# Optimization experiments

Hardware: AMD Instinct MI355X
Metric: run time of the kernel (lower is better)

The kernel has to match this reference:

```python
import jax, jax.numpy as jnp
import numpy as np

D = 512       # d_model
H = 8         # n_heads
HD = D // H   # head_dim
LYR = 4       # number_of_layers
PMT = 20      # pmt_len
L = 2048      # decode / target length (src_len - pmt_len)
BS = 1
DOUT = 3      # d_output (3 coding classes)
DFF = 4 * D
EPS = 1e-5


def layer_norm(x, g, b):
    m = jnp.mean(x, axis=-1, keepdims=True)
    v = jnp.mean((x - m) ** 2, axis=-1, keepdims=True)
    return (x - m) * jax.lax.rsqrt(v + EPS) * g + b


def rope(x):
    # x: (b, h, s, hd); half-split rotary with base 10000, positions = arange(s)
    half = x.shape[-1] // 2
    pos = jnp.arange(x.shape[2], dtype=jnp.float32)
    inv_freq = 1.0 / (10000.0 ** (jnp.arange(half, dtype=jnp.float32) / half))
    ang = pos[:, None] * inv_freq[None, :]          # (s, half)
    cos = jnp.cos(ang)[None, None]                  # (1,1,s,half)
    sin = jnp.sin(ang)[None, None]
    x1, x2 = x[..., :half], x[..., half:]
    return jnp.concatenate([x1 * cos - x2 * sin, x1 * sin + x2 * cos], axis=-1)


def mha(xq, xkv, wqkv, bqkv, wo, bo, key_mask, causal):
    # xq: (b, sq, D), xkv: (b, sk, D); key_mask: (b, sk) with 1=valid
    b, sq, _ = xq.shape
    sk = xkv.shape[1]
    q = xq @ wqkv[:, :D] + bqkv[:D]
    kv = xkv @ wqkv[:, D:] + bqkv[D:]
    k, v = kv[..., :D], kv[..., D:]
    q = q.reshape(b, sq, H, HD).transpose(0, 2, 1, 3)   # (b,h,sq,hd)
    k = k.reshape(b, sk, H, HD).transpose(0, 2, 1, 3)
    v = v.reshape(b, sk, H, HD).transpose(0, 2, 1, 3)
    q = rope(q)
    k = rope(k)
    scores = jnp.einsum('bhqd,bhkd->bhqk', q, k) / jnp.sqrt(jnp.float32(HD))
    scores = scores + jnp.where(key_mask[:, None, None, :] > 0, 0.0, -1e9)
    if causal:
        cm = jnp.tril(jnp.ones((sq, sk), dtype=bool))
        scores = jnp.where(cm[None, None], scores, -1e9)
    attn = jax.nn.softmax(scores, axis=-1)
    out = jnp.einsum('bhqk,bhkd->bhqd', attn, v)
    out = out.transpose(0, 2, 1, 3).reshape(b, sq, D)
    return out @ wo + bo


def setup_inputs() -> dict:
    key = jax.random.key(0)
    ks = jax.random.split(key, 16)
    s = 0.02
    p = lambda i, shape: jax.random.normal(ks[i], shape, jnp.float32) * s
    return {
        'trg_inputs': jax.random.normal(ks[0], (BS, L, DOUT), jnp.float32),
        'src_rep': jax.random.normal(ks[1], (BS, PMT + L, D), jnp.float32),
        'src_mask': jnp.ones((BS, L), jnp.float32),
        'emb_w': p(2, (DOUT, D)), 'emb_b': jnp.zeros((D,), jnp.float32),
        'sa_wqkv': p(3, (LYR, D, 3 * D)), 'sa_bqkv': jnp.zeros((LYR, 3 * D), jnp.float32),
        'sa_wo': p(4, (LYR, D, D)), 'sa_bo': jnp.zeros((LYR, D), jnp.float32),
        'ca_wqkv': p(5, (LYR, D, 3 * D)), 'ca_bqkv': jnp.zeros((LYR, 3 * D), jnp.float32),
        'ca_wo': p(6, (LYR, D, D)), 'ca_bo': jnp.zeros((LYR, D), jnp.float32),
        'ffn_w1': p(7, (LYR, D, DFF)), 'ffn_b1': jnp.zeros((LYR, DFF), jnp.float32),
        'ffn_w2': p(8, (LYR, DFF, D)), 'ffn_b2': jnp.zeros((LYR, D), jnp.float32),
        'ln_g': jnp.ones((LYR, 3, D), jnp.float32), 'ln_b': jnp.zeros((LYR, 3, D), jnp.float32),
        'lnf_g': jnp.ones((D,), jnp.float32), 'lnf_b': jnp.zeros((D,), jnp.float32),
        'gen_w': p(9, (D, DOUT)), 'gen_b': jnp.zeros((DOUT,), jnp.float32),
    }


def reference(trg_inputs, src_rep, src_mask, emb_w, emb_b, sa_wqkv, sa_bqkv, sa_wo, sa_bo,
              ca_wqkv, ca_bqkv, ca_wo, ca_bo, ffn_w1, ffn_b1, ffn_w2, ffn_b2,
              ln_g, ln_b, lnf_g, lnf_b, gen_w, gen_b):
    srb = src_rep[:, PMT:, :]                       # (bs, L, D)
    x = trg_inputs @ emb_w + emb_b                  # (bs, L, D)
    trg_mask = src_mask                             # parallel mode: trg_mask = src_mask
    for li in range(LYR):
        h = layer_norm(x, ln_g[li, 0], ln_b[li, 0])
        x = x + mha(h, h, sa_wqkv[li], sa_bqkv[li], sa_wo[li], sa_bo[li], trg_mask, causal=True)
        h = layer_norm(x, ln_g[li, 1], ln_b[li, 1])
        x = x + mha(h, srb, ca_wqkv[li], ca_bqkv[li], ca_wo[li], ca_bo[li], src_mask, causal=False)
        h = layer_norm(x, ln_g[li, 2], ln_b[li, 2])
        x = x + (jax.nn.relu(h @ ffn_w1[li] + ffn_b1[li]) @ ffn_w2[li] + ffn_b2[li])
    x = layer_norm(x, lnf_g, lnf_b)
    return x @ gen_w + gen_b                        # logits (bs, L, 3)
```

## Files before the change

### kernel.cpp

```cpp
#include <hip/hip_runtime.h>
#include <hip/hip_bf16.h>

#define SEQ 2048
#define DM 512
#define NHEAD 8
#define HDIM 64
#define DFFN 2048
#define PMTN 20

typedef __bf16 bf16x8 __attribute__((ext_vector_type(8)));
typedef float f32x4 __attribute__((ext_vector_type(4)));
typedef unsigned short u16x8 __attribute__((ext_vector_type(8)));

__device__ __forceinline__ float wave_sum(float v) {
#pragma unroll
  for (int off = 32; off; off >>= 1) v += __shfl_xor(v, off);
  return v;
}

__device__ __forceinline__ unsigned short f2b(float x) {
  __hip_bfloat16 h = __float2bfloat16(x);
  return *(unsigned short*)&h;
}

__device__ __forceinline__ void gll16(const __hip_bfloat16* g, __hip_bfloat16* l) {
  __builtin_amdgcn_global_load_lds(
      (const __attribute__((address_space(1))) unsigned int*)(g),
      (__attribute__((address_space(3))) unsigned int*)(l), 16, 0, 0);
}

__global__ __launch_bounds__(256) void embed_kernel(
    const float* __restrict__ trg, const float* __restrict__ w,
    const float* __restrict__ b, float* __restrict__ X) {
  int idx = blockIdx.x * 256 + threadIdx.x;
  int r = idx >> 9, c = idx & 511;
  float t0 = trg[r * 3 + 0], t1 = trg[r * 3 + 1], t2 = trg[r * 3 + 2];
  X[idx] = t0 * w[c] + t1 * w[512 + c] + t2 * w[1024 + c] + b[c];
}

__global__ __launch_bounds__(256) void cast_bf16_kernel(
    const float* __restrict__ in, __hip_bfloat16* __restrict__ out) {
  int i = blockIdx.x * 256 + threadIdx.x;
  out[i] = __float2bfloat16(in[i]);
}

__global__ __launch_bounds__(256) void rope_table_kernel(float2* __restrict__ rt) {
  int idx = blockIdx.x * 256 + threadIdx.x;
  int row = idx >> 5, i = idx & 31;
  float inv = __expf(-(float)i * (9.210340371976184f / 32.f));
  float sn, cs;
  sincosf((float)row * inv, &sn, &cs);
  rt[idx] = make_float2(cs, sn);
}

__global__ __launch_bounds__(256) void mbias_kernel(
    const float* __restrict__ mask, float* __restrict__ mb,
    int* __restrict__ mtflag) {
  int i = blockIdx.x * 256 + threadIdx.x;
  bool masked = !(mask[i] > 0.f);
  mb[i] = masked ? -8.0e9f : 0.f;
  unsigned long long any = __ballot(masked);
  if ((threadIdx.x & 63) == 0) mtflag[i >> 6] = (any != 0ull) ? 1 : 0;
}

__global__ __launch_bounds__(256) void ln_bf16_kernel(
    const float* __restrict__ x, const float* __restrict__ g,
    const float* __restrict__ b, __hip_bfloat16* __restrict__ o) {
  int row = blockIdx.x * 4 + (threadIdx.x >> 6);
  int lane = threadIdx.x & 63;
  const float* xr = x + (long)row * DM;
  float v[8];
  float s = 0.f;
#pragma unroll
  for (int j = 0; j < 8; j++) { v[j] = xr[lane + 64 * j]; s += v[j]; }
  s = wave_sum(s);
  float mean = s * (1.f / DM);
  float q = 0.f;
#pragma unroll
  for (int j = 0; j < 8; j++) { float d = v[j] - mean; q += d * d; }
  q = wave_sum(q);
  float r = rsqrtf(q * (1.f / DM) + 1e-5f);
  __hip_bfloat16* orow = o + (long)row * DM;
#pragma unroll
  for (int j = 0; j < 8; j++) {
    int c = lane + 64 * j;
    orow[c] = __float2bfloat16((v[j] - mean) * r * g[c] + b[c]);
  }
}

__global__ __launch_bounds__(256) void ln_f32_kernel(
    const float* __restrict__ x, const float* __restrict__ g,
    const float* __restrict__ b, float* __restrict__ o) {
  int row = blockIdx.x * 4 + (threadIdx.x >> 6);
  int lane = threadIdx.x & 63;
  const float* xr = x + (long)row * DM;
  float v[8];
  float s = 0.f;
#pragma unroll
  for (int j = 0; j < 8; j++) { v[j] = xr[lane + 64 * j]; s += v[j]; }
  s = wave_sum(s);
  float mean = s * (1.f / DM);
  float q = 0.f;
#pragma unroll
  for (int j = 0; j < 8; j++) { float d = v[j] - mean; q += d * d; }
  q = wave_sum(q);
  float r = rsqrtf(q * (1.f / DM) + 1e-5f);
  float* orow = o + (long)row * DM;
#pragma unroll
  for (int j = 0; j < 8; j++) {
    int c = lane + 64 * j;
    orow[c] = (v[j] - mean) * r * g[c] + b[c];
  }
}

__global__ __launch_bounds__(256) void transpose_layer_kernel(
    const float* __restrict__ wqkv, const float* __restrict__ wo,
    const float* __restrict__ cwqkv, const float* __restrict__ cwo,
    const float* __restrict__ w1, const float* __restrict__ w2,
    __hip_bfloat16* __restrict__ Wt) {
  int b = blockIdx.x;
  const float* W;
  __hip_bfloat16* O;
  int Kd, Nd;
  if (b < 192)      { W = wqkv;  O = Wt + 0;       Kd = 512;  Nd = 1536; }
  else if (b < 256) { W = wo;    O = Wt + 786432;  Kd = 512;  Nd = 512;  b -= 192; }
  else if (b < 448) { W = cwqkv; O = Wt + 1048576; Kd = 512;  Nd = 1536; b -= 256; }
  else if (b < 512) { W = cwo;   O = Wt + 1835008; Kd = 512;  Nd = 512;  b -= 448; }
  else if (b < 768) { W = w1;    O = Wt + 2097152; Kd = 512;  Nd = 2048; b -= 512; }
  else              { W = w2;    O = Wt + 3145728; Kd = 2048; Nd = 512;  b -= 768; }
  int tn = Nd >> 6;
  int k0 = (b / tn) * 64, n0 = (b % tn) * 64;
  __shared__ float T[64][65];
  int t = threadIdx.x;
  int rr = t >> 4, c4 = (t & 15) * 4;
#pragma unroll
  for (int p = 0; p < 4; p++) {
    int row = rr + p * 16;
    float4 v = *(const float4*)(W + (long)(k0 + row) * Nd + n0 + c4);
    T[row][c4 + 0] = v.x; T[row][c4 + 1] = v.y;
    T[row][c4 + 2] = v.z; T[row][c4 + 3] = v.w;
  }
  __syncthreads();
#pragma unroll
  for (int p = 0; p < 4; p++) {
    int row = rr + p * 16;
    ushort4 pk;
    pk.x = f2b(T[c4 + 0][row]); pk.y = f2b(T[c4 + 1][row]);
    pk.z = f2b(T[c4 + 2][row]); pk.w = f2b(T[c4 + 3][row]);
    *(ushort4*)(O + (long)(n0 + row) * Kd + k0 + c4) = pk;
  }
}

__global__ __launch_bounds__(256) void gemm_bf16_64(
    const __hip_bfloat16* __restrict__ A, int lda,
    const __hip_bfloat16* __restrict__ A2,
    const __hip_bfloat16* __restrict__ Bt, int ldb,
    const float* __restrict__ bias,
    const float* __restrict__ residual,
    float* __restrict__ Cf, __hip_bfloat16* __restrict__ Cb, int ldc,
    int K, int relu, int mode, const float2* __restrict__ rt,
    __hip_bfloat16* __restrict__ Qp, __hip_bfloat16* __restrict__ Kp,
    __hip_bfloat16* __restrict__ Vtp) {
  __shared__ __attribute__((aligned(16))) __hip_bfloat16 As[2][4096];
  __shared__ __attribute__((aligned(16))) __hip_bfloat16 Bs[2][4096];
  const int t = threadIdx.x;
  const int bx = blockIdx.x;
  const int nrow = bx * 64, m0 = blockIdx.y * 64;
  const int ptype = (mode == 0) ? 3 : (nrow < 512 ? 0 : (nrow < 1024 ? 1 : 2));
  const int head = (nrow >> 6) & 7;
  const __hip_bfloat16* Ause = (mode == 2 && bx >= 8) ? A2 : A;

  const int w = t >> 6, lane = t & 63;
  const int wr = w >> 1, wc = w & 1;
  const int fr = lane & 15, fk = lane >> 4;
  const int r0 = t & 63, c0 = t >> 6;
  const __hip_bfloat16* Arow = Ause + (long)(m0 + r0) * lda;
  const __hip_bfloat16* Brow = Bt + (long)(nrow + r0) * ldb;

  uint4 ra0 = *(const uint4*)(Arow + c0 * 8);
  uint4 ra1 = *(const uint4*)(Arow + (c0 + 4) * 8);
  uint4 rb0 = *(const uint4*)(Brow + c0 * 8);
  uint4 rb1 = *(const uint4*)(Brow + (c0 + 4) * 8);
  *(uint4*)(&As[0][(c0 * 64 + r0) * 8]) = ra0;
  *(uint4*)(&As[0][((c0 + 4) * 64 + r0) * 8]) = ra1;
  *(uint4*)(&Bs[0][(c0 * 64 + r0) * 8]) = rb0;
  *(uint4*)(&Bs[0][((c0 + 4) * 64 + r0) * 8]) = rb1;
  __syncthreads();

  f32x4 acc[2][2] = {};
  const int NK = K >> 6;
  for (int ks = 0; ks < NK; ++ks) {
    const int cur = ks & 1;
    if (ks + 1 < NK) {
      const int ko = (ks + 1) << 6;
      ra0 = *(const uint4*)(Arow + ko + c0 * 8);
      ra1 = *(const uint4*)(Arow + ko + (c0 + 4) * 8);
      rb0 = *(const uint4*)(Brow + ko + c0 * 8);
      rb1 = *(const uint4*)(Brow + ko + (c0 + 4) * 8);
    }
#pragma unroll
    for (int kk = 0; kk < 2; ++kk) {
      const int kc = kk * 4 + fk;
      bf16x8 a0 = *(const bf16x8*)(&As[cur][(kc * 64 + wr * 32 + fr) * 8]);
      bf16x8 a1 = *(const bf16x8*)(&As[cur][(kc * 64 + wr * 32 + 16 + fr) * 8]);
      bf16x8 b0 = *(const bf16x8*)(&Bs[cur][(kc * 64 + wc * 32 + fr) * 8]);
      bf16x8 b1 = *(const bf16x8*)(&Bs[cur][(kc * 64 + wc * 32 + 16 + fr) * 8]);
      acc[0][0] = __builtin_amdgcn_mfma_f32_16x16x32_bf16(a0, b0, acc[0][0], 0, 0, 0);
      acc[0][1] = __builtin_amdgcn_mfma_f32_16x16x32_bf16(a0, b1, acc[0][1], 0, 0, 0);
      acc[1][0] = __builtin_amdgcn_mfma_f32_16x16x32_bf16(a1, b0, acc[1][0], 0, 0, 0);
      acc[1][1] = __builtin_amdgcn_mfma_f32_16x16x32_bf16(a1, b1, acc[1][1], 0, 0, 0);
    }
    if (ks + 1 < NK) {
      const int nxt = cur ^ 1;
      *(uint4*)(&As[nxt][(c0 * 64 + r0) * 8]) = ra0;
      *(uint4*)(&As[nxt][((c0 + 4) * 64 + r0) * 8]) = ra1;
      *(uint4*)(&Bs[nxt][(c0 * 64 + r0) * 8]) = rb0;
      *(uint4*)(&Bs[nxt][((c0 + 4) * 64 + r0) * 8]) = rb1;
    }
    __syncthreads();
  }

  if (ptype == 3) {
#pragma unroll
    for (int m = 0; m < 2; ++m)
#pragma unroll
      for (int n = 0; n < 2; ++n)
#pragma unroll
        for (int j = 0; j < 4; ++j) {
          int r = m0 + wr * 32 + m * 16 + fk * 4 + j;
          int c = nrow + wc * 32 + n * 16 + fr;
          float v = acc[m][n][j] + bias[c];
          if (relu) v = fmaxf(v, 0.f);
          if (residual) v += residual[(long)r * ldc + c];
          if (Cf) Cf[(long)r * ldc + c] = v;
          if (Cb) Cb[(long)r * ldc + c] = __float2bfloat16(v);
        }
    return;
  }

  float* Lt = (float*)As;
#pragma unroll
  for (int m = 0; m < 2; ++m)
#pragma unroll
    for (int n = 0; n < 2; ++n)
#pragma unroll
      for (int j = 0; j < 4; ++j) {
        int rl = wr * 32 + m * 16 + fk * 4 + j;
        int cl = wc * 32 + n * 16 + fr;
        Lt[rl * 64 + (cl ^ (rl & 31))] = acc[m][n][j] + bias[nrow + cl];
      }
  __syncthreads();

  if (ptype == 2) {
    const int d = t >> 2, sc = (t & 3) * 16;
    u16x8 o0, o1;
#pragma unroll
    for (int s = 0; s < 8; s++) {
      o0[s] = f2b(Lt[(sc + s) * 64 + (d ^ ((sc + s) & 31))]);
      o1[s] = f2b(Lt[(sc + 8 + s) * 64 + (d ^ ((sc + 8 + s) & 31))]);
    }
    __hip_bfloat16* dst = Vtp + ((long)(head * 64 + d)) * SEQ + m0 + sc;
    *(u16x8*)dst = o0;
    *(u16x8*)(dst + 8) = o1;
  } else {
    const int r = t >> 2, i0 = (t & 3) * 8;
    const float2* rp = rt + (long)(m0 + r) * 32 + i0;
    u16x8 lo, hi;
#pragma unroll
    for (int p = 0; p < 8; p++) {
      float a = Lt[r * 64 + ((i0 + p) ^ (r & 31))];
      float b = Lt[r * 64 + ((i0 + p + 32) ^ (r & 31))];
      float2 cs = rp[p];
      lo[p] = f2b(a * cs.x - b * cs.y);
      hi[p] = f2b(a * cs.y + b * cs.x);
    }
    __hip_bfloat16* dst =
        (ptype == 0 ? Qp : Kp) + ((long)head * SEQ + m0 + r) * 64 + i0;
    *(u16x8*)dst = lo;
    *(u16x8*)(dst + 32) = hi;
  }
}

__global__ __launch_bounds__(256) void attn_part_kernel(
    const __hip_bfloat16* __restrict__ Qp, const __hip_bfloat16* __restrict__ Kp,
    const __hip_bfloat16* __restrict__ Vtp, const float* __restrict__ mbias,
    const int* __restrict__ mtflag,
    __hip_bfloat16* __restrict__ Op, float* __restrict__ Ml,
    int causal, int csz) {
  const int qt = blockIdx.x, ch = blockIdx.y, head = blockIdx.z;
  const int kv0 = ch * csz;
  if (causal && kv0 > qt * 64 + 63) return;
  const int kvlen = causal ? min(csz, qt * 64 + 64 - kv0) : csz;
  const int nt = (kvlen + 63) >> 6;

  __shared__ __attribute__((aligned(16))) __hip_bfloat16 Ks[4096];
  __shared__ __attribute__((aligned(16))) __hip_bfloat16 Vs[4096];
  __shared__ __attribute__((aligned(16))) __hip_bfloat16 Ps[4096];
  const int t = threadIdx.x, w = t >> 6, lane = t & 63;
  const int fr = lane & 15, fk = lane >> 4;
  const int qr = qt * 64 + w * 16 + fr;
  const int wq0 = qt * 64 + w * 16;
  const float SCL = 0.18033688011112042f;

  bf16x8 qa0, qa1;
  {
    const __hip_bfloat16* qp = Qp + ((long)head * SEQ + qr) * 64 + fk * 8;
    qa0 = *(const bf16x8*)qp;
    qa1 = *(const bf16x8*)(qp + 32);
  }
  const __hip_bfloat16* Kh = Kp + (long)head * SEQ * 64;
  const __hip_bfloat16* Vh = Vtp + (long)head * 64 * SEQ;

  float m_i = -3e38f, l_i = 0.f;
  f32x4 o_[4] = {};
  const int sw2 = (fr & 7) << 4;

  for (int tile = 0; tile < nt; ++tile) {
    const int kb = kv0 + tile * 64;
    __syncthreads();
    {
      const __hip_bfloat16* src = Kh + (long)(kb + (t & 63)) * 64 + (t >> 6) * 8;
      gll16(src, Ks + t * 8);
      gll16(src + 32, Ks + t * 8 + 2048);
    }
    {
      const __hip_bfloat16* src = Vh + (long)(t & 63) * SEQ + kb + (t >> 6) * 8;
      gll16(src, Vs + t * 8);
      gll16(src + 32, Vs + t * 8 + 2048);
    }
    __syncthreads();

    const bool need = !causal || (kb <= wq0 + 15);
    if (need) {
      const bool diag = causal && (kb + 63 > wq0);
      const bool hasmask = mtflag[kb >> 6] != 0;

      f32x4 sacc[4];
      __builtin_amdgcn_s_setprio(1);
#pragma unroll
      for (int n = 0; n < 4; n++) {
        bf16x8 ka0 = *(const bf16x8*)(Ks + fk * 512 + (n * 16 + fr) * 8);
        bf16x8 ka1 = *(const bf16x8*)(Ks + (4 + fk) * 512 + (n * 16 + fr) * 8);
        f32x4 zz = {};
        zz = __builtin_amdgcn_mfma_f32_16x16x32_bf16(ka0, qa0, zz, 0, 0, 0);
        sacc[n] = __builtin_amdgcn_mfma_f32_16x16x32_bf16(ka1, qa1, zz, 0, 0, 0);
      }
      __builtin_amdgcn_s_setprio(0);

      float sv[4][4];
      float rm = -3e38f;
#pragma unroll
      for (int n = 0; n < 4; n++) {
        const int ka = kb + n * 16 + fk * 4;
        if (hasmask) {
          float4 mb = *(const float4*)(mbias + ka);
          sv[n][0] = sacc[n][0] + mb.x;
          sv[n][1] = sacc[n][1] + mb.y;
          sv[n][2] = sacc[n][2] + mb.z;
          sv[n][3] = sacc[n][3] + mb.w;
        } else {
          sv[n][0] = sacc[n][0]; sv[n][1] = sacc[n][1];
          sv[n][2] = sacc[n][2]; sv[n][3] = sacc[n][3];
        }
        if (diag) {
#pragma unroll
          for (int j = 0; j < 4; j++)
            if (ka + j > qr) sv[n][j] = -3e38f;
        }
#pragma unroll
        for (int j = 0; j < 4; j++) rm = fmaxf(rm, sv[n][j]);
      }
      rm = fmaxf(rm, __shfl_xor(rm, 16));
      rm = fmaxf(rm, __shfl_xor(rm, 32));
      if (!__all(rm <= m_i)) {
        float nm = fmaxf(m_i, rm);
        float f = exp2f((m_i - nm) * SCL);
        l_i *= f;
#pragma unroll
        for (int n = 0; n < 4; n++) o_[n] *= f;
        m_i = nm;
      }
      float ps = 0.f;
#pragma unroll
      for (int n = 0; n < 4; n++) {
        float p0 = exp2f((sv[n][0] - m_i) * SCL);
        float p1 = exp2f((sv[n][1] - m_i) * SCL);
        float p2 = exp2f((sv[n][2] - m_i) * SCL);
        float p3 = exp2f((sv[n][3] - m_i) * SCL);
        ps += (p0 + p1) + (p2 + p3);
        ushort4 pk4;
        pk4.x = f2b(p0); pk4.y = f2b(p1); pk4.z = f2b(p2); pk4.w = f2b(p3);
        *(ushort4*)((char*)Ps + ((w * 2048 + fr * 128 + (n * 16 + fk * 4) * 2) ^ sw2)) = pk4;
      }
      ps += __shfl_xor(ps, 16);
      ps += __shfl_xor(ps, 32);
      l_i += ps;

      __builtin_amdgcn_s_setprio(1);
#pragma unroll
      for (int s = 0; s < 2; s++) {
        bf16x8 pb = *(const bf16x8*)((char*)Ps + ((w * 2048 + fr * 128 + s * 64 + fk * 16) ^ sw2));
#pragma unroll
        for (int n = 0; n < 4; n++) {
          bf16x8 va = *(const bf16x8*)(Vs + (s * 4 + fk) * 512 + (n * 16 + fr) * 8);
          o_[n] = __builtin_amdgcn_mfma_f32_16x16x32_bf16(va, pb, o_[n], 0, 0, 0);
        }
      }
      __builtin_amdgcn_s_setprio(0);
    }
  }

  const long bid = ((long)head * 32 + qt) * gridDim.y + ch;
  __hip_bfloat16* Ob = Op + bid * 4096;
#pragma unroll
  for (int n = 0; n < 4; n++) {
    ushort4 ov;
    ov.x = f2b(o_[n][0]); ov.y = f2b(o_[n][1]);
    ov.z = f2b(o_[n][2]); ov.w = f2b(o_[n][3]);
    *(ushort4*)(Ob + (w * 16 + fr) * 64 + n * 16 + fk * 4) = ov;
  }
  if (fk == 0) {
    float2 ml = make_float2(m_i, l_i);
    *(float2*)(Ml + bid * 128 + (w * 16 + fr) * 2) = ml;
  }
}

__global__ __launch_bounds__(256) void attn_combine_kernel(
    const __hip_bfloat16* __restrict__ Op, const float* __restrict__ Ml,
    __hip_bfloat16* __restrict__ O, int ldo, int causal, int csz, int nch) {
  const int qt = blockIdx.x, head = blockIdx.y;
  const int nc = causal ? min(nch, (qt * 64 + 63) / csz + 1) : nch;
  const int t = threadIdx.x;
  const int row = t >> 2, c16 = (t & 3) * 16;
  const long bid0 = ((long)head * 32 + qt) * nch;
  const float SCL = 0.18033688011112042f;
  float M = -3e38f;
  for (int c = 0; c < nc; c++) M = fmaxf(M, Ml[(bid0 + c) * 128 + row * 2]);
  float L = 0.f;
  float acc[16] = {};
  for (int c = 0; c < nc; c++) {
    float2 ml = *(const float2*)(Ml + (bid0 + c) * 128 + row * 2);
    float wg = exp2f((ml.x - M) * SCL);
    L += wg * ml.y;
    const __hip_bfloat16* base = Op + (bid0 + c) * 4096 + row * 64 + c16;
    bf16x8 a = *(const bf16x8*)base;
    bf16x8 b = *(const bf16x8*)(base + 8);
#pragma unroll
    for (int e = 0; e < 8; e++) {
      acc[e] += wg * (float)a[e];
      acc[8 + e] += wg * (float)b[e];
    }
  }
  float invL = 1.f / fmaxf(L, 1e-20f);
  u16x8 o0, o1;
#pragma unroll
  for (int e = 0; e < 8; e++) {
    o0[e] = f2b(acc[e] * invL);
    o1[e] = f2b(acc[8 + e] * invL);
  }
  __hip_bfloat16* orow = O + (long)(qt * 64 + row) * ldo + head * 64 + c16;
  *(u16x8*)orow = o0;
  *(u16x8*)(orow + 8) = o1;
}

__global__ __launch_bounds__(64) void gen_kernel(
    const float* __restrict__ h, const float* __restrict__ gw,
    const float* __restrict__ gb, float* __restrict__ out) {
  int row = blockIdx.x, lane = threadIdx.x;
  float a0 = 0.f, a1 = 0.f, a2 = 0.f;
  for (int k = lane; k < DM; k += 64) {
    float x = h[(long)row * DM + k];
    a0 = fmaf(x, gw[k * 3 + 0], a0);
    a1 = fmaf(x, gw[k * 3 + 1], a1);
    a2 = fmaf(x, gw[k * 3 + 2], a2);
  }
  a0 = wave_sum(a0);
  a1 = wave_sum(a1);
  a2 = wave_sum(a2);
  if (lane == 0) {
    out[row * 3 + 0] = a0 + gb[0];
    out[row * 3 + 1] = a1 + gb[1];
    out[row * 3 + 2] = a2 + gb[2];
  }
}

extern "C" void kernel_launch(void* const* d_in, const int* in_sizes, int n_in,
                              void* d_out, int out_size, void* d_ws, size_t ws_size,
                              hipStream_t stream) {
  const float* trg      = (const float*)d_in[0];
  const float* src_rep  = (const float*)d_in[1];
  const float* src_mask = (const float*)d_in[2];
  const float* emb_w    = (const float*)d_in[3];
  const float* emb_b    = (const float*)d_in[4];
  const float* sa_wqkv  = (const float*)d_in[5];
  const float* sa_bqkv  = (const float*)d_in[6];
  const float* sa_wo    = (const float*)d_in[7];
  const float* sa_bo    = (const float*)d_in[8];
  const float* ca_wqkv  = (const float*)d_in[9];
  const float* ca_bqkv  = (const float*)d_in[10];
  const float* ca_wo    = (const float*)d_in[11];
  const float* ca_bo    = (const float*)d_in[12];
  const float* ffn_w1   = (const float*)d_in[13];
  const float* ffn_b1   = (const float*)d_in[14];
  const float* ffn_w2   = (const float*)d_in[15];
  const float* ffn_b2   = (const float*)d_in[16];
  const float* ln_g     = (const float*)d_in[17];
  const float* ln_b     = (const float*)d_in[18];
  const float* lnf_g    = (const float*)d_in[19];
  const float* lnf_b    = (const float*)d_in[20];
  const float* gen_w    = (const float*)d_in[21];
  const float* gen_b    = (const float*)d_in[22];

  const float* srb = src_rep + (long)PMTN * DM;

  char* wsb = (char*)d_ws;
  float*          X    = (float*)wsb;
  __hip_bfloat16* Hb   = (__hip_bfloat16*)(wsb + (4ul << 20));
  __hip_bfloat16* MID  = (__hip_bfloat16*)(wsb + (6ul << 20));
  __hip_bfloat16* Op   = MID;
  float*          Hf   = (float*)MID;
  __hip_bfloat16* AO   = (__hip_bfloat16*)(wsb + (14ul << 20));
  __hip_bfloat16* SRBb = (__hip_bfloat16*)(wsb + (16ul << 20));
  float2*         rt   = (float2*)(wsb + (18ul << 20));
  float*          mbias= (float*)(wsb + (18ul << 20) + 524288);
  int*            mtfl = (int*)(wsb + (18ul << 20) + 532480);
  float*          Ml   = (float*)(wsb + (19ul << 20));
  __hip_bfloat16* Qp   = (__hip_bfloat16*)(wsb + (20ul << 20));
  __hip_bfloat16* Kp   = (__hip_bfloat16*)(wsb + (22ul << 20));
  __hip_bfloat16* Vtp  = (__hip_bfloat16*)(wsb + (24ul << 20));
  __hip_bfloat16* Wt   = (__hip_bfloat16*)(wsb + (26ul << 20));

  const int nch = 4;
  const int csz = SEQ / nch;

  embed_kernel<<<(SEQ * DM) / 256, 256, 0, stream>>>(trg, emb_w, emb_b, X);
  cast_bf16_kernel<<<(SEQ * DM) / 256, 256, 0, stream>>>(srb, SRBb);
  rope_table_kernel<<<256, 256, 0, stream>>>(rt);
  mbias_kernel<<<8, 256, 0, stream>>>(src_mask, mbias, mtfl);

  __hip_bfloat16* wqkvT  = Wt + 0;
  __hip_bfloat16* woT    = Wt + 786432;
  __hip_bfloat16* cwqkvT = Wt + 1048576;
  __hip_bfloat16* cwoT   = Wt + 1835008;
  __hip_bfloat16* w1T    = Wt + 2097152;
  __hip_bfloat16* w2T    = Wt + 3145728;

  for (int li = 0; li < 4; li++) {
    transpose_layer_kernel<<<1024, 256, 0, stream>>>(
        sa_wqkv + (long)li * DM * 3 * DM, sa_wo + (long)li * DM * DM,
        ca_wqkv + (long)li * DM * 3 * DM, ca_wo + (long)li * DM * DM,
        ffn_w1 + (long)li * DM * DFFN, ffn_w2 + (long)li * DFFN * DM, Wt);

    const float* bqkv  = sa_bqkv + (long)li * 3 * DM;
    const float* bo    = sa_bo + (long)li * DM;
    const float* cbqkv = ca_bqkv + (long)li * 3 * DM;
    const float* cbo   = ca_bo + (long)li * DM;
    const float* b1    = ffn_b1 + (long)li * DFFN;
    const float* b2    = ffn_b2 + (long)li * DM;
    const float* g0  = ln_g + (long)(li * 3 + 0) * DM;
    const float* bb0 = ln_b + (long)(li * 3 + 0) * DM;
    const float* g1  = ln_g + (long)(li * 3 + 1) * DM;
    const float* bb1 = ln_b + (long)(li * 3 + 1) * DM;
    const float* g2  = ln_g + (long)(li * 3 + 2) * DM;
    const float* bb2 = ln_b + (long)(li * 3 + 2) * DM;

    ln_bf16_kernel<<<512, 256, 0, stream>>>(X, g0, bb0, Hb);
    gemm_bf16_64<<<dim3(24, 32), 256, 0, stream>>>(
        Hb, DM, nullptr, wqkvT, DM, bqkv, nullptr, nullptr, nullptr, DM,
        DM, 0, 1, rt, Qp, Kp, Vtp);
    attn_part_kernel<<<dim3(32, nch, 8), 256, 0, stream>>>(
        Qp, Kp, Vtp, mbias, mtfl, Op, Ml, 1, csz);
    attn_combine_kernel<<<dim3(32, 8), 256, 0, stream>>>(
        Op, Ml, AO, DM, 1, csz, nch);
    gemm_bf16_64<<<dim3(8, 32), 256, 0, stream>>>(
        AO, DM, nullptr, woT, DM, bo, X, X, nullptr, DM,
        DM, 0, 0, nullptr, nullptr, nullptr, nullptr);

    ln_bf16_kernel<<<512, 256, 0, stream>>>(X, g1, bb1, Hb);
    gemm_bf16_64<<<dim3(24, 32), 256, 0, stream>>>(
        Hb, DM, SRBb, cwqkvT, DM, cbqkv, nullptr, nullptr, nullptr, DM,
        DM, 0, 2, rt, Qp, Kp, Vtp);
    attn_part_kernel<<<dim3(32, nch, 8), 256, 0, stream>>>(
        Qp, Kp, Vtp, mbias, mtfl, Op, Ml, 0, csz);
    attn_combine_kernel<<<dim3(32, 8), 256, 0, stream>>>(
        Op, Ml, AO, DM, 0, csz, nch);
    gemm_bf16_64<<<dim3(8, 32), 256, 0, stream>>>(
        AO, DM, nullptr, cwoT, DM, cbo, X, X, nullptr, DM,
        DM, 0, 0, nullptr, nullptr, nullptr, nullptr);

    ln_bf16_kernel<<<512, 256, 0, stream>>>(X, g2, bb2, Hb);
    gemm_bf16_64<<<dim3(32, 32), 256, 0, stream>>>(
        Hb, DM, nullptr, w1T, DM, b1, nullptr, nullptr, MID, DFFN,
        DM, 1, 0, nullptr, nullptr, nullptr, nullptr);
    gemm_bf16_64<<<dim3(8, 32), 256, 0, stream>>>(
        MID, DFFN, nullptr, w2T, DFFN, b2, X, X, nullptr, DM,
        DFFN, 0, 0, nullptr, nullptr, nullptr, nullptr);
  }

  ln_f32_kernel<<<512, 256, 0, stream>>>(X, lnf_g, lnf_b, Hf);
  gen_kernel<<<SEQ, 64, 0, stream>>>(Hf, gen_w, gen_b, (float*)d_out);
}
```

Baseline: 760.8 us.

## Double-buffer K/V tiles in attention and fuse final layernorm with generator

The attention partial kernel now keeps two LDS buffers for K and V. The next tile's async global-to-LDS load is issued right after the barrier, so it overlaps the MFMA work on the current tile, and one barrier per iteration is removed. Separately, the final layernorm and the 3-way output projection run in one kernel, which avoids writing and re-reading a full fp32 activation buffer and saves a launch. The cost is more LDS per block (40KB instead of 24KB), which may lower attention occupancy.

```diff
diff --git a/kernel.cpp b/kernel.cpp
--- a/kernel.cpp
+++ b/kernel.cpp
@@ -88,9 +88,10 @@
   }
 }
 
-__global__ __launch_bounds__(256) void ln_f32_kernel(
+__global__ __launch_bounds__(256) void ln_gen_kernel(
     const float* __restrict__ x, const float* __restrict__ g,
-    const float* __restrict__ b, float* __restrict__ o) {
+    const float* __restrict__ b, const float* __restrict__ gw,
+    const float* __restrict__ gb, float* __restrict__ out) {
   int row = blockIdx.x * 4 + (threadIdx.x >> 6);
   int lane = threadIdx.x & 63;
   const float* xr = x + (long)row * DM;
@@ -105,11 +106,22 @@
   for (int j = 0; j < 8; j++) { float d = v[j] - mean; q += d * d; }
   q = wave_sum(q);
   float r = rsqrtf(q * (1.f / DM) + 1e-5f);
-  float* orow = o + (long)row * DM;
+  float a0 = 0.f, a1 = 0.f, a2 = 0.f;
 #pragma unroll
   for (int j = 0; j < 8; j++) {
     int c = lane + 64 * j;
-    orow[c] = (v[j] - mean) * r * g[c] + b[c];
+    float nv = (v[j] - mean) * r * g[c] + b[c];
+    a0 = fmaf(nv, gw[c * 3 + 0], a0);
+    a1 = fmaf(nv, gw[c * 3 + 1], a1);
+    a2 = fmaf(nv, gw[c * 3 + 2], a2);
+  }
+  a0 = wave_sum(a0);
+  a1 = wave_sum(a1);
+  a2 = wave_sum(a2);
+  if (lane == 0) {
+    out[row * 3 + 0] = a0 + gb[0];
+    out[row * 3 + 1] = a1 + gb[1];
+    out[row * 3 + 2] = a2 + gb[2];
   }
 }
 
@@ -293,8 +305,8 @@
   const int kvlen = causal ? min(csz, qt * 64 + 64 - kv0) : csz;
   const int nt = (kvlen + 63) >> 6;
 
-  __shared__ __attribute__((aligned(16))) __hip_bfloat16 Ks[4096];
-  __shared__ __attribute__((aligned(16))) __hip_bfloat16 Vs[4096];
+  __shared__ __attribute__((aligned(16))) __hip_bfloat16 Ks[2][4096];
+  __shared__ __attribute__((aligned(16))) __hip_bfloat16 Vs[2][4096];
   __shared__ __attribute__((aligned(16))) __hip_bfloat16 Ps[4096];
   const int t = threadIdx.x, w = t >> 6, lane = t & 63;
   const int fr = lane & 15, fk = lane >> 4;
@@ -310,26 +322,35 @@
   }
   const __hip_bfloat16* Kh = Kp + (long)head * SEQ * 64;
   const __hip_bfloat16* Vh = Vtp + (long)head * 64 * SEQ;
+  const int skr = t & 63, skc = t >> 6;
 
   float m_i = -3e38f, l_i = 0.f;
   f32x4 o_[4] = {};
   const int sw2 = (fr & 7) << 4;
 
+  {
+    const __hip_bfloat16* ksrc = Kh + (long)(kv0 + skr) * 64 + skc * 8;
+    gll16(ksrc, Ks[0] + t * 8);
+    gll16(ksrc + 32, Ks[0] + t * 8 + 2048);
+    const __hip_bfloat16* vsrc = Vh + (long)skr * SEQ + kv0 + skc * 8;
+    gll16(vsrc, Vs[0] + t * 8);
+    gll16(vsrc + 32, Vs[0] + t * 8 + 2048);
+  }
+
   for (int tile = 0; tile < nt; ++tile) {
+    __syncthreads();
+    const int cur = tile & 1;
+    if (tile + 1 < nt) {
+      const int kb1 = kv0 + (tile + 1) * 64;
+      const int nxt = cur ^ 1;
+      const __hip_bfloat16* ksrc = Kh + (long)(kb1 + skr) * 64 + skc * 8;
+      gll16(ksrc, Ks[nxt] + t * 8);
+      gll16(ksrc + 32, Ks[nxt] + t * 8 + 2048);
+      const __hip_bfloat16* vsrc = Vh + (long)skr * SEQ + kb1 + skc * 8;
+      gll16(vsrc, Vs[nxt] + t * 8);
+      gll16(vsrc + 32, Vs[nxt] + t * 8 + 2048);
+    }
     const int kb = kv0 + tile * 64;
-    __syncthreads();
-    {
-      const __hip_bfloat16* src = Kh + (long)(kb + (t & 63)) * 64 + (t >> 6) * 8;
-      gll16(src, Ks + t * 8);
-      gll16(src + 32, Ks + t * 8 + 2048);
-    }
-    {
-      const __hip_bfloat16* src = Vh + (long)(t & 63) * SEQ + kb + (t >> 6) * 8;
-      gll16(src, Vs + t * 8);
-      gll16(src + 32, Vs + t * 8 + 2048);
-    }
-    __syncthreads();
-
     const bool need = !causal || (kb <= wq0 + 15);
     if (need) {
       const bool diag = causal && (kb + 63 > wq0);
@@ -339,8 +360,8 @@
       __builtin_amdgcn_s_setprio(1);
 #pragma unroll
       for (int n = 0; n < 4; n++) {
-        bf16x8 ka0 = *(const bf16x8*)(Ks + fk * 512 + (n * 16 + fr) * 8);
-        bf16x8 ka1 = *(const bf16x8*)(Ks + (4 + fk) * 512 + (n * 16 + fr) * 8);
+        bf16x8 ka0 = *(const bf16x8*)(Ks[cur] + fk * 512 + (n * 16 + fr) * 8);
+        bf16x8 ka1 = *(const bf16x8*)(Ks[cur] + (4 + fk) * 512 + (n * 16 + fr) * 8);
         f32x4 zz = {};
         zz = __builtin_amdgcn_mfma_f32_16x16x32_bf16(ka0, qa0, zz, 0, 0, 0);
         sacc[n] = __builtin_amdgcn_mfma_f32_16x16x32_bf16(ka1, qa1, zz, 0, 0, 0);
@@ -402,7 +423,7 @@
         bf16x8 pb = *(const bf16x8*)((char*)Ps + ((w * 2048 + fr * 128 + s * 64 + fk * 16) ^ sw2));
 #pragma unroll
         for (int n = 0; n < 4; n++) {
-          bf16x8 va = *(const bf16x8*)(Vs + (s * 4 + fk) * 512 + (n * 16 + fr) * 8);
+          bf16x8 va = *(const bf16x8*)(Vs[cur] + (s * 4 + fk) * 512 + (n * 16 + fr) * 8);
           o_[n] = __builtin_amdgcn_mfma_f32_16x16x32_bf16(va, pb, o_[n], 0, 0, 0);
         }
       }
@@ -461,27 +482,6 @@
   __hip_bfloat16* orow = O + (long)(qt * 64 + row) * ldo + head * 64 + c16;
   *(u16x8*)orow = o0;
   *(u16x8*)(orow + 8) = o1;
-}
-
-__global__ __launch_bounds__(64) void gen_kernel(
-    const float* __restrict__ h, const float* __restrict__ gw,
-    const float* __restrict__ gb, float* __restrict__ out) {
-  int row = blockIdx.x, lane = threadIdx.x;
-  float a0 = 0.f, a1 = 0.f, a2 = 0.f;
-  for (int k = lane; k < DM; k += 64) {
-    float x = h[(long)row * DM + k];
-    a0 = fmaf(x, gw[k * 3 + 0], a0);
-    a1 = fmaf(x, gw[k * 3 + 1], a1);
-    a2 = fmaf(x, gw[k * 3 + 2], a2);
-  }
-  a0 = wave_sum(a0);
-  a1 = wave_sum(a1);
-  a2 = wave_sum(a2);
-  if (lane == 0) {
-    out[row * 3 + 0] = a0 + gb[0];
-    out[row * 3 + 1] = a1 + gb[1];
-    out[row * 3 + 2] = a2 + gb[2];
-  }
 }
 
 extern "C" void kernel_launch(void* const* d_in, const int* in_sizes, int n_in,
@@ -518,7 +518,6 @@
   __hip_bfloat16* Hb   = (__hip_bfloat16*)(wsb + (4ul << 20));
   __hip_bfloat16* MID  = (__hip_bfloat16*)(wsb + (6ul << 20));
   __hip_bfloat16* Op   = MID;
-  float*          Hf   = (float*)MID;
   __hip_bfloat16* AO   = (__hip_bfloat16*)(wsb + (14ul << 20));
   __hip_bfloat16* SRBb = (__hip_bfloat16*)(wsb + (16ul << 20));
   float2*         rt   = (float2*)(wsb + (18ul << 20));
@@ -597,6 +596,6 @@
         DFFN, 0, 0, nullptr, nullptr, nullptr, nullptr);
   }
 
-  ln_f32_kernel<<<512, 256, 0, stream>>>(X, lnf_g, lnf_b, Hf);
-  gen_kernel<<<SEQ, 64, 0, stream>>>(Hf, gen_w, gen_b, (float*)d_out);
-}
+  ln_gen_kernel<<<512, 256, 0, stream>>>(X, lnf_g, lnf_b, gen_w, gen_b,
+                                         (float*)d_out);
+}
```

Result: no change. 758.8 us (-0.3%).
